# Performance work log

Hardware: AMD Instinct MI355X
Metric: run time of the kernel (lower is better)

The kernel has to match this reference:

```python
import jax, jax.numpy as jnp
import numpy as np

T_REF = 160.0
MU_MIN, MU_MAX = 0.1, 1.3
N_CYCLES, BATCH = 150, 65536
PARAM_NAMES = ['a0', 'a_T', 'a_mu', 'a_mu2', 'c0', 'c_mu', 'c_T', 's0', 's_mu', 's_T',
               'j0', 'j_mu', 'j_T', 'v0', 'v_mu', 'mu0_base', 'mu0_T']
PARAM_INIT = {'a0': 2.0, 'a_T': -0.1, 'a_mu': -1.0, 'a_mu2': 0.5, 'c0': 0.01, 'c_mu': -0.02,
              'c_T': 0.001, 's0': -3.0, 's_mu': 1.0, 's_T': 0.1, 'j0': 0.5, 'j_mu': -1.0,
              'j_T': 0.02, 'v0': -1.5, 'v_mu': 0.5, 'mu0_base': 0.12, 'mu0_T': 0.005}


def setup_inputs() -> dict:
    key = jax.random.key(0)
    k_u, k_n = jax.random.split(key)
    params = jnp.asarray(np.array([PARAM_INIT[n] for n in PARAM_NAMES], dtype=np.float32))
    T = jnp.asarray(200.0, dtype=jnp.float32)  # temperature in degC
    u = jax.random.uniform(k_u, (N_CYCLES, BATCH), dtype=jnp.float32)      # mixture choice
    noise = jax.random.normal(k_n, (N_CYCLES, BATCH), dtype=jnp.float32)   # Gaussian draw
    return {"params": params, "T": T, "u": u, "noise": noise}


def reference(params, T, u, noise):
    # Batched, scan-based version of InteractiveGallingModelV6.simulate().
    (a0, a_T, a_mu, a_mu2, c0, c_mu, c_T, s0, s_mu, s_T,
     j0, j_mu, j_T, v0, v_mu, mu0_base, mu0_T) = [params[i] for i in range(17)]
    dT = T - T_REF
    B = u.shape[1]
    mu0 = jnp.clip(mu0_base + mu0_T * dT, MU_MIN, MU_MAX)
    mu_init = jnp.full((B,), mu0, dtype=u.dtype)

    def step(mu, un):
        u_t, n_t = un
        pi = jax.nn.sigmoid(a0 + a_T * dT + a_mu * mu + a_mu2 * mu * mu)
        d1 = c0 + c_mu * mu + c_T * dT
        sigma1 = jax.nn.softplus(s0 + s_mu * mu + s_T * dT)
        d2 = j0 + j_mu * mu + j_T * dT
        sigma2 = jax.nn.softplus(v0 + v_mu * mu)
        is_stay = u_t < pi
        component = (~is_stay).astype(mu.dtype)
        delta_mu = jnp.where(is_stay, d1 + sigma1 * n_t, d2 + sigma2 * n_t)
        mu_next = jnp.clip(mu + delta_mu, MU_MIN, MU_MAX)
        ys = jnp.stack([mu_next, component,
                        jnp.broadcast_to(pi, mu.shape),
                        jnp.broadcast_to(d1, mu.shape),
                        jnp.broadcast_to(sigma1, mu.shape),
                        jnp.broadcast_to(d2, mu.shape),
                        jnp.broadcast_to(sigma2, mu.shape)])  # [7, B]
        return mu_next, ys

    _, ys = jax.lax.scan(step, mu_init, (u, noise))  # [N, 7, B]
    # [7, N, B]: mu_hist, component_hist, pi_hist, d1_hist, sigma1_hist, d2_hist, sigma2_hist
    return jnp.transpose(ys, (1, 0, 2))
```

## Files before the change

### kernel.cpp

```cpp
#include <hip/hip_runtime.h>
#include <cmath>

constexpr int   NCY   = 150;
constexpr int   BATCH = 65536;
constexpr float MU_MIN = 0.1f;
constexpr float MU_MAX = 1.3f;
constexpr float T_REFC = 160.0f;

__device__ __forceinline__ float softplus_stable(float x) {
    return fmaxf(x, 0.0f) + log1pf(expf(-fabsf(x)));
}

__global__ __launch_bounds__(256)
void galling_sim_kernel(const float* __restrict__ params,
                        const float* __restrict__ Tptr,
                        const float* __restrict__ u,
                        const float* __restrict__ noise,
                        float* __restrict__ out)
{
#pragma clang fp contract(off)

    const int b = blockIdx.x * blockDim.x + threadIdx.x;

    const float a0   = params[0],  a_T  = params[1],  a_mu = params[2],  a_mu2 = params[3];
    const float c0   = params[4],  c_mu = params[5],  c_T  = params[6];
    const float s0   = params[7],  s_mu = params[8],  s_T  = params[9];
    const float j0   = params[10], j_mu = params[11], j_T  = params[12];
    const float v0   = params[13], v_mu = params[14];
    const float mu0_base = params[15], mu0_T = params[16];

    const float dT = Tptr[0] - T_REFC;

    const float A  = a0 + a_T * dT;
    const float ct = c_T * dT;
    const float st = s_T * dT;
    const float jt = j_T * dT;

    float mu = fminf(fmaxf(mu0_base + mu0_T * dT, MU_MIN), MU_MAX);

    const float* up  = u     + b;
    const float* npp = noise + b;
    float*       o   = out   + b;
    const size_t NB  = (size_t)NCY * (size_t)BATCH;

    float u_a = up[0];
    float n_a = npp[0];
    float u_b = up[(size_t)BATCH];
    float n_b = npp[(size_t)BATCH];

    for (int t = 0; t < NCY; ++t) {
        const float u_cur = u_a;
        const float n_cur = n_a;
        u_a = u_b; n_a = n_b;
        const int tn = (t + 2 < NCY) ? (t + 2) : (NCY - 1);
        u_b = up[(size_t)tn * BATCH];
        n_b = npp[(size_t)tn * BATCH];

        const float x_pi = (A + a_mu * mu) + (a_mu2 * mu) * mu;
        const float pi   = 1.0f / (1.0f + expf(-x_pi));

        const float d1 = (c0 + c_mu * mu) + ct;
        const float sigma1 = softplus_stable((s0 + s_mu * mu) + st);
        const float d2 = (j0 + j_mu * mu) + jt;
        const float sigma2 = softplus_stable(v0 + v_mu * mu);

        const bool  is_stay   = u_cur < pi;
        const float component = is_stay ? 0.0f : 1.0f;
        const float delta_mu  = is_stay ? (d1 + sigma1 * n_cur)
                                        : (d2 + sigma2 * n_cur);
        const float mu_next   = fminf(fmaxf(mu + delta_mu, MU_MIN), MU_MAX);

        const size_t base = (size_t)t * (size_t)BATCH;
        o[0 * NB + base] = mu_next;
        o[1 * NB + base] = component;
        o[2 * NB + base] = pi;
        o[3 * NB + base] = d1;
        o[4 * NB + base] = sigma1;
        o[5 * NB + base] = d2;
        o[6 * NB + base] = sigma2;

        mu = mu_next;
    }
}

extern "C" void kernel_launch(void* const* d_in, const int* in_sizes, int n_in,
                              void* d_out, int out_size, void* d_ws, size_t ws_size,
                              hipStream_t stream) {
    const float* params = (const float*)d_in[0];
    const float* Tptr   = (const float*)d_in[1];
    const float* u      = (const float*)d_in[2];
    const float* noise  = (const float*)d_in[3];
    float*       out    = (float*)d_out;

    dim3 block(256);
    dim3 grid(BATCH / 256);
    galling_sim_kernel<<<grid, block, 0, stream>>>(params, Tptr, u, noise, out);
}
```

Before: 408.0 us.

## Split scan into serial mu pass and time-parallel stats recompute kernel

The simulation is split into two kernels. The first runs the serial recurrence with a deeper 4-step prefetch of u and noise and writes only the mu history. The second kernel, gridded over batch and 4-step time chunks, reads mu back, recomputes pi, d1, sigma1, d2 and sigma2 and the component, and writes the other six outputs. This is meant to move most of the store traffic off the serial 256-block kernel and into a kernel with far more parallelism, at the cost of an extra launch, rereading mu and u, and computing the transcendentals twice.

```diff
diff --git a/kernel.cpp b/kernel.cpp
--- a/kernel.cpp
+++ b/kernel.cpp
@@ -1,25 +1,45 @@
 #include <hip/hip_runtime.h>
 #include <cmath>
 
-constexpr int   NCY   = 150;
-constexpr int   BATCH = 65536;
-constexpr float MU_MIN = 0.1f;
-constexpr float MU_MAX = 1.3f;
-constexpr float T_REFC = 160.0f;
+constexpr int    NCY   = 150;
+constexpr int    BATCH = 65536;
+constexpr size_t NB    = (size_t)NCY * (size_t)BATCH;
+constexpr float  MU_MIN = 0.1f;
+constexpr float  MU_MAX = 1.3f;
+constexpr float  T_REFC = 160.0f;
 
 __device__ __forceinline__ float softplus_stable(float x) {
+#pragma clang fp contract(off)
     return fmaxf(x, 0.0f) + log1pf(expf(-fabsf(x)));
 }
 
+struct StepStats { float pi, d1, s1, d2, s2; };
+
+__device__ __forceinline__ StepStats step_stats(float mu,
+        float A, float a_mu, float a_mu2,
+        float c0, float c_mu, float ct,
+        float s0, float s_mu, float st,
+        float j0, float j_mu, float jt,
+        float v0, float v_mu) {
+#pragma clang fp contract(off)
+    StepStats r;
+    const float x_pi = (A + a_mu * mu) + (a_mu2 * mu) * mu;
+    r.pi = 1.0f / (1.0f + expf(-x_pi));
+    r.d1 = (c0 + c_mu * mu) + ct;
+    r.s1 = softplus_stable((s0 + s_mu * mu) + st);
+    r.d2 = (j0 + j_mu * mu) + jt;
+    r.s2 = softplus_stable(v0 + v_mu * mu);
+    return r;
+}
+
 __global__ __launch_bounds__(256)
-void galling_sim_kernel(const float* __restrict__ params,
-                        const float* __restrict__ Tptr,
-                        const float* __restrict__ u,
-                        const float* __restrict__ noise,
-                        float* __restrict__ out)
+void galling_p1(const float* __restrict__ params,
+                const float* __restrict__ Tptr,
+                const float* __restrict__ u,
+                const float* __restrict__ noise,
+                float* __restrict__ out)
 {
 #pragma clang fp contract(off)
-
     const int b = blockIdx.x * blockDim.x + threadIdx.x;
 
     const float a0   = params[0],  a_T  = params[1],  a_mu = params[2],  a_mu2 = params[3];
@@ -30,7 +50,6 @@
     const float mu0_base = params[15], mu0_T = params[16];
 
     const float dT = Tptr[0] - T_REFC;
-
     const float A  = a0 + a_T * dT;
     const float ct = c_T * dT;
     const float st = s_T * dT;
@@ -40,46 +59,88 @@
 
     const float* up  = u     + b;
     const float* npp = noise + b;
-    float*       o   = out   + b;
-    const size_t NB  = (size_t)NCY * (size_t)BATCH;
 
-    float u_a = up[0];
-    float n_a = npp[0];
-    float u_b = up[(size_t)BATCH];
-    float n_b = npp[(size_t)BATCH];
+    float uf[4], nf[4];
+#pragma unroll
+    for (int i = 0; i < 4; ++i) {
+        uf[i] = up [(size_t)i * BATCH];
+        nf[i] = npp[(size_t)i * BATCH];
+    }
 
+#pragma unroll 4
     for (int t = 0; t < NCY; ++t) {
-        const float u_cur = u_a;
-        const float n_cur = n_a;
-        u_a = u_b; n_a = n_b;
-        const int tn = (t + 2 < NCY) ? (t + 2) : (NCY - 1);
-        u_b = up[(size_t)tn * BATCH];
-        n_b = npp[(size_t)tn * BATCH];
+        const float u_cur = uf[t & 3];
+        const float n_cur = nf[t & 3];
+        const int tp = (t + 4 < NCY) ? (t + 4) : (NCY - 1);
+        uf[t & 3] = up [(size_t)tp * BATCH];
+        nf[t & 3] = npp[(size_t)tp * BATCH];
 
-        const float x_pi = (A + a_mu * mu) + (a_mu2 * mu) * mu;
-        const float pi   = 1.0f / (1.0f + expf(-x_pi));
+        const StepStats s = step_stats(mu, A, a_mu, a_mu2, c0, c_mu, ct,
+                                       s0, s_mu, st, j0, j_mu, jt, v0, v_mu);
+        const bool  stay    = u_cur < s.pi;
+        const float delta   = stay ? (s.d1 + s.s1 * n_cur) : (s.d2 + s.s2 * n_cur);
+        const float mu_next = fminf(fmaxf(mu + delta, MU_MIN), MU_MAX);
 
-        const float d1 = (c0 + c_mu * mu) + ct;
-        const float sigma1 = softplus_stable((s0 + s_mu * mu) + st);
-        const float d2 = (j0 + j_mu * mu) + jt;
-        const float sigma2 = softplus_stable(v0 + v_mu * mu);
+        out[(size_t)t * BATCH + b] = mu_next;
+        mu = mu_next;
+    }
+}
 
-        const bool  is_stay   = u_cur < pi;
-        const float component = is_stay ? 0.0f : 1.0f;
-        const float delta_mu  = is_stay ? (d1 + sigma1 * n_cur)
-                                        : (d2 + sigma2 * n_cur);
-        const float mu_next   = fminf(fmaxf(mu + delta_mu, MU_MIN), MU_MAX);
+__global__ __launch_bounds__(256)
+void galling_p2(const float* __restrict__ params,
+                const float* __restrict__ Tptr,
+                const float* __restrict__ u,
+                float* __restrict__ out)
+{
+#pragma clang fp contract(off)
+    const int b  = blockIdx.x * blockDim.x + threadIdx.x;
+    const int t0 = blockIdx.y * 4;
+    const int nt = (t0 + 4 <= NCY) ? 4 : (NCY - t0);
 
-        const size_t base = (size_t)t * (size_t)BATCH;
-        o[0 * NB + base] = mu_next;
-        o[1 * NB + base] = component;
-        o[2 * NB + base] = pi;
-        o[3 * NB + base] = d1;
-        o[4 * NB + base] = sigma1;
-        o[5 * NB + base] = d2;
-        o[6 * NB + base] = sigma2;
+    const float a0   = params[0],  a_T  = params[1],  a_mu = params[2],  a_mu2 = params[3];
+    const float c0   = params[4],  c_mu = params[5],  c_T  = params[6];
+    const float s0   = params[7],  s_mu = params[8],  s_T  = params[9];
+    const float j0   = params[10], j_mu = params[11], j_T  = params[12];
+    const float v0   = params[13], v_mu = params[14];
+    const float mu0_base = params[15], mu0_T = params[16];
 
-        mu = mu_next;
+    const float dT = Tptr[0] - T_REFC;
+    const float A  = a0 + a_T * dT;
+    const float ct = c_T * dT;
+    const float st = s_T * dT;
+    const float jt = j_T * dT;
+
+    const float* mu_hist = out;
+
+    float mu_prev = (t0 == 0)
+        ? fminf(fmaxf(mu0_base + mu0_T * dT, MU_MIN), MU_MAX)
+        : mu_hist[(size_t)(t0 - 1) * BATCH + b];
+
+    float muc[4], uc[4];
+#pragma unroll
+    for (int i = 0; i < 4; ++i) {
+        if (i < nt) {
+            const size_t base = (size_t)(t0 + i) * BATCH + b;
+            muc[i] = mu_hist[base];
+            uc[i]  = u[base];
+        }
+    }
+
+#pragma unroll
+    for (int i = 0; i < 4; ++i) {
+        if (i < nt) {
+            const StepStats s = step_stats(mu_prev, A, a_mu, a_mu2, c0, c_mu, ct,
+                                           s0, s_mu, st, j0, j_mu, jt, v0, v_mu);
+            const float comp = (uc[i] < s.pi) ? 0.0f : 1.0f;
+            const size_t base = (size_t)(t0 + i) * BATCH + b;
+            out[1 * NB + base] = comp;
+            out[2 * NB + base] = s.pi;
+            out[3 * NB + base] = s.d1;
+            out[4 * NB + base] = s.s1;
+            out[5 * NB + base] = s.d2;
+            out[6 * NB + base] = s.s2;
+            mu_prev = muc[i];
+        }
     }
 }
 
@@ -92,7 +153,6 @@
     const float* noise  = (const float*)d_in[3];
     float*       out    = (float*)d_out;
 
-    dim3 block(256);
-    dim3 grid(BATCH / 256);
-    galling_sim_kernel<<<grid, block, 0, stream>>>(params, Tptr, u, noise, out);
+    galling_p1<<<dim3(BATCH / 256), dim3(256), 0, stream>>>(params, Tptr, u, noise, out);
+    galling_p2<<<dim3(BATCH / 256, (NCY + 3) / 4), dim3(256), 0, stream>>>(params, Tptr, u, out);
 }
```

After: 418.9 us. +2.7%, slower.
